# Kernel tuning notes

Measured on AMD Instinct MI355X. Metric: run time of the kernel, lower is better.

The kernel has to match this reference:

```python
import jax, jax.numpy as jnp
import numpy as np

N_NODES = 200000
N_EDGES = 3200000
N_GRAPHS = 64
IN_DIM, HIDDEN, OUT_DIM = 128, 16, 64


def setup_inputs() -> dict:
    key = jax.random.key(0)
    ks = jax.random.split(key, 5)
    x = jax.random.normal(ks[0], (N_NODES, IN_DIM), dtype=jnp.float32)
    edge_index = jax.random.randint(ks[1], (2, N_EDGES), 0, N_NODES, dtype=jnp.int64)
    batch = jnp.sort(jax.random.randint(ks[2], (N_NODES,), 0, N_GRAPHS, dtype=jnp.int64))
    W1 = jax.random.normal(ks[3], (IN_DIM, HIDDEN), dtype=jnp.float32) * (1.0 / np.sqrt(IN_DIM))
    W2 = jax.random.normal(ks[4], (HIDDEN, OUT_DIM), dtype=jnp.float32) * (1.0 / np.sqrt(HIDDEN))
    b1 = jnp.zeros((HIDDEN,), jnp.float32)
    b2 = jnp.zeros((OUT_DIM,), jnp.float32)
    return {"x": x, "edge_index": edge_index, "batch": batch,
            "W1": W1, "b1": b1, "W2": W2, "b2": b2, "training": 0}


def _gcn_conv(x, W, b, row, col, n_nodes):
    # PyG GCNConv: add-self-loop symmetric normalization, transform then
    # gather-from-row / scatter-add-to-col.  (row, col) already include self-loops.
    h = x @ W                                             # [N, out]
    deg = jnp.zeros((n_nodes,), h.dtype).at[col].add(1.0)  # degree incl. self-loop (>=1)
    dinv = deg ** -0.5
    norm = dinv[row] * dinv[col]                          # [E+N]
    out = jnp.zeros((n_nodes, W.shape[1]), h.dtype).at[col].add(h[row] * norm[:, None])
    return out + b


def reference(x, edge_index, batch, W1, b1, W2, b2, training):
    n = x.shape[0]
    loops = jnp.arange(n, dtype=edge_index.dtype)
    row = jnp.concatenate([edge_index[0], loops])
    col = jnp.concatenate([edge_index[1], loops])
    h = _gcn_conv(x, W1, b1, row, col, n)
    h = jax.nn.relu(h)
    # F.dropout with training=False is identity (reference is deterministic)
    h = _gcn_conv(h, W2, b2, row, col, n)
    # per-graph sum pooling: replaces the Python torch.where loop
    graph_embeds = jax.ops.segment_sum(h, batch, num_segments=N_GRAPHS)
    return graph_embeds
```

## Files before the change

kernel.cpp:

```cpp
#include <hip/hip_runtime.h>


#define TPB 256
#define CHUNK 4096
#define BK_SHIFT 9
#define NPB 512

__device__ __forceinline__ float bf2f(unsigned short u) {
    union { unsigned int i; float f; } v; v.i = ((unsigned int)u) << 16; return v.f;
}
__device__ __forceinline__ unsigned short f2bf(float f) {
    union { float f; unsigned int i; } v; v.f = f;
    unsigned int r = v.i + 0x7fff + ((v.i >> 16) & 1);
    return (unsigned short)(r >> 16);
}

__global__ __launch_bounds__(TPB) void hist_kernel(const int* __restrict__ col,
                                                   int* __restrict__ counts,
                                                   int E, int nblk, int nbuck) {
    __shared__ int hist[512];
    int t = threadIdx.x;
    for (int i = t; i < nbuck; i += TPB) hist[i] = 0;
    __syncthreads();
    int e0 = blockIdx.x * CHUNK;
    for (int i = t; i < CHUNK; i += TPB) {
        int e = e0 + i;
        if (e < E) atomicAdd(&hist[col[e] >> BK_SHIFT], 1);
    }
    __syncthreads();
    for (int i = t; i < nbuck; i += TPB) counts[i * nblk + blockIdx.x] = hist[i];
}

__global__ __launch_bounds__(TPB) void scan1_kernel(const int* __restrict__ in,
                                                    int* __restrict__ out,
                                                    int* __restrict__ bsum, int L) {
    __shared__ int s[TPB];
    int t = threadIdx.x;
    int i = blockIdx.x * TPB + t;
    int d = (i < L) ? in[i] : 0;
    s[t] = d; __syncthreads();
    for (int off = 1; off < TPB; off <<= 1) {
        int v = (t >= off) ? s[t - off] : 0;
        __syncthreads();
        s[t] += v;
        __syncthreads();
    }
    if (i < L) out[i] = s[t] - d;
    if (t == TPB - 1) bsum[blockIdx.x] = s[t];
}

__global__ __launch_bounds__(1024) void scan2_kernel(int* __restrict__ bsum, int nb) {
    __shared__ int s[1024];
    int t = threadIdx.x;
    int i0 = t * 2, i1 = t * 2 + 1;
    int v0 = (i0 < nb) ? bsum[i0] : 0;
    int v1 = (i1 < nb) ? bsum[i1] : 0;
    int pv = v0 + v1;
    s[t] = pv; __syncthreads();
    for (int off = 1; off < 1024; off <<= 1) {
        int u = (t >= off) ? s[t - off] : 0;
        __syncthreads();
        s[t] += u;
        __syncthreads();
    }
    int exc = s[t] - pv;
    if (i0 < nb) bsum[i0] = exc;
    if (i1 < nb) bsum[i1] = exc + v0;
}

__device__ __forceinline__ int cbase_at(const int* counts, const int* bsum, int f) {
    return counts[f] + bsum[f >> 8];
}

__global__ __launch_bounds__(TPB) void s1c_gemm_kernel(
        const int* __restrict__ row, const int* __restrict__ col,
        const int* __restrict__ counts, const int* __restrict__ bsum,
        int E, int nblk, int nbuck,
        int* __restrict__ bucketed,
        const float* __restrict__ x, const float* __restrict__ W1,
        unsigned short* __restrict__ h1b, int N, int nbg) {
    __shared__ int cur[NPB];
    __shared__ float w1s[128 * 16];
    int b = (int)blockIdx.x, t = threadIdx.x;
    int M = min(nblk, nbg);
    int role, id;
    if (b < 2 * M) { role = b & 1; id = b >> 1; }
    else           { role = (nblk > nbg) ? 0 : 1; id = b - M; }

    if (role == 0) {
        for (int i = t; i < nbuck; i += TPB)
            cur[i] = cbase_at(counts, bsum, i * nblk + id);
        __syncthreads();
        int e0 = id * CHUNK;
        for (int i = t; i < CHUNK; i += TPB) {
            int e = e0 + i;
            if (e < E) {
                int c = col[e];
                int pos = atomicAdd(&cur[c >> BK_SHIFT], 1);
                bucketed[pos] = ((c & (NPB - 1)) << 18) | row[e];
            }
        }
        return;
    }
    for (int i = t; i < 128 * 16; i += TPB) w1s[i] = W1[i];
    __syncthreads();
    int n = id * TPB + t;
    if (n >= N) return;
    const float4* xr = (const float4*)(x + (size_t)n * 128);
    float acc[16];
#pragma unroll
    for (int k = 0; k < 16; ++k) acc[k] = 0.f;
#pragma unroll 1
    for (int g = 0; g < 8; g += 2) {
        float4 vA0 = xr[g * 4 + 0], vA1 = xr[g * 4 + 1];
        float4 vA2 = xr[g * 4 + 2], vA3 = xr[g * 4 + 3];
        float4 vB0 = xr[g * 4 + 4], vB1 = xr[g * 4 + 5];
        float4 vB2 = xr[g * 4 + 6], vB3 = xr[g * 4 + 7];
        float xva[16] = {vA0.x, vA0.y, vA0.z, vA0.w, vA1.x, vA1.y, vA1.z, vA1.w,
                         vA2.x, vA2.y, vA2.z, vA2.w, vA3.x, vA3.y, vA3.z, vA3.w};
        float xvb[16] = {vB0.x, vB0.y, vB0.z, vB0.w, vB1.x, vB1.y, vB1.z, vB1.w,
                         vB2.x, vB2.y, vB2.z, vB2.w, vB3.x, vB3.y, vB3.z, vB3.w};
#pragma unroll
        for (int cc = 0; cc < 16; ++cc) {
            const float4* w4 = (const float4*)&w1s[(g * 16 + cc) * 16];
            float4 wa = w4[0], wb = w4[1], wc = w4[2], wd = w4[3];
            float xc = xva[cc];
            acc[0]  = fmaf(xc, wa.x, acc[0]);  acc[1]  = fmaf(xc, wa.y, acc[1]);
            acc[2]  = fmaf(xc, wa.z, acc[2]);  acc[3]  = fmaf(xc, wa.w, acc[3]);
            acc[4]  = fmaf(xc, wb.x, acc[4]);  acc[5]  = fmaf(xc, wb.y, acc[5]);
            acc[6]  = fmaf(xc, wb.z, acc[6]);  acc[7]  = fmaf(xc, wb.w, acc[7]);
            acc[8]  = fmaf(xc, wc.x, acc[8]);  acc[9]  = fmaf(xc, wc.y, acc[9]);
            acc[10] = fmaf(xc, wc.z, acc[10]); acc[11] = fmaf(xc, wc.w, acc[11]);
            acc[12] = fmaf(xc, wd.x, acc[12]); acc[13] = fmaf(xc, wd.y, acc[13]);
            acc[14] = fmaf(xc, wd.z, acc[14]); acc[15] = fmaf(xc, wd.w, acc[15]);
        }
#pragma unroll
        for (int cc = 0; cc < 16; ++cc) {
            const float4* w4 = (const float4*)&w1s[((g + 1) * 16 + cc) * 16];
            float4 wa = w4[0], wb = w4[1], wc = w4[2], wd = w4[3];
            float xc = xvb[cc];
            acc[0]  = fmaf(xc, wa.x, acc[0]);  acc[1]  = fmaf(xc, wa.y, acc[1]);
            acc[2]  = fmaf(xc, wa.z, acc[2]);  acc[3]  = fmaf(xc, wa.w, acc[3]);
            acc[4]  = fmaf(xc, wb.x, acc[4]);  acc[5]  = fmaf(xc, wb.y, acc[5]);
            acc[6]  = fmaf(xc, wb.z, acc[6]);  acc[7]  = fmaf(xc, wb.w, acc[7]);
            acc[8]  = fmaf(xc, wc.x, acc[8]);  acc[9]  = fmaf(xc, wc.y, acc[9]);
            acc[10] = fmaf(xc, wc.z, acc[10]); acc[11] = fmaf(xc, wc.w, acc[11]);
            acc[12] = fmaf(xc, wd.x, acc[12]); acc[13] = fmaf(xc, wd.y, acc[13]);
            acc[14] = fmaf(xc, wd.z, acc[14]); acc[15] = fmaf(xc, wd.w, acc[15]);
        }
    }
    unsigned int u[8];
#pragma unroll
    for (int j = 0; j < 8; ++j)
        u[j] = (unsigned int)f2bf(acc[2 * j]) | ((unsigned int)f2bf(acc[2 * j + 1]) << 16);
    uint4* o = (uint4*)(h1b + (size_t)n * 16);
    o[0] = make_uint4(u[0], u[1], u[2], u[3]);
    o[1] = make_uint4(u[4], u[5], u[6], u[7]);
}

__global__ __launch_bounds__(TPB) void sort_kernel(
        const int* __restrict__ bucketed,
        const int* __restrict__ counts, const int* __restrict__ bsum,
        int E, int nblk, int nbuck,
        int* __restrict__ csr, int* __restrict__ offs, float* __restrict__ dinv,
        const unsigned short* __restrict__ h1b, unsigned short* __restrict__ h1p, int N) {
    __shared__ int lhist[NPB];
    __shared__ int part[TPB];
    __shared__ float sdinv[NPB];
    int bk = blockIdx.x, t = threadIdx.x;
    int n0 = bk << BK_SHIFT;
    int n1 = min(n0 + NPB, N);
    int e0 = cbase_at(counts, bsum, bk * nblk);
    int e1 = (bk + 1 < nbuck) ? cbase_at(counts, bsum, (bk + 1) * nblk) : E;

    lhist[t] = 0; lhist[t + TPB] = 0;
    __syncthreads();
    for (int i = e0 + t; i < e1; i += TPB)
        atomicAdd(&lhist[bucketed[i] >> 18], 1);
    __syncthreads();

    int base = t * 2;
    int c0 = lhist[base], c1 = lhist[base + 1];
    int s = c0 + c1;
    part[t] = s;
    __syncthreads();
    for (int off = 1; off < TPB; off <<= 1) {
        int v = (t >= off) ? part[t - off] : 0;
        __syncthreads();
        part[t] += v;
        __syncthreads();
    }
    int o0 = e0 + part[t] - s;
    int o1 = o0 + c0;
    lhist[base] = o0; lhist[base + 1] = o1;
    sdinv[base]     = rsqrtf((float)c0 + 1.0f);
    sdinv[base + 1] = rsqrtf((float)c1 + 1.0f);
    int n = n0 + base;
    if (n + 0 < N) { offs[n + 0] = o0; dinv[n + 0] = sdinv[base]; }
    if (n + 1 < N) { offs[n + 1] = o1; dinv[n + 1] = sdinv[base + 1]; }
    __syncthreads();

    for (int i = e0 + t; i < e1; i += TPB) {
        int v = bucketed[i];
        int pos = atomicAdd(&lhist[v >> 18], 1);
        csr[pos] = v & 0x3FFFF;
    }
    int nq = (n1 - n0) * 4;
    for (int i = t; i < nq; i += TPB) {
        float dv = sdinv[i >> 2];
        uint2 u = ((const uint2*)h1b)[(size_t)n0 * 4 + i];
        float f0 = bf2f((unsigned short)(u.x & 0xffff));
        float f1 = bf2f((unsigned short)(u.x >> 16));
        float f2 = bf2f((unsigned short)(u.y & 0xffff));
        float f3 = bf2f((unsigned short)(u.y >> 16));
        ((ushort4*)h1p)[(size_t)n0 * 4 + i] =
            make_ushort4(f2bf(f0 * dv), f2bf(f1 * dv), f2bf(f2 * dv), f2bf(f3 * dv));
    }
    if (bk == 0 && t == 0) offs[N] = E;
}

__global__ __launch_bounds__(TPB) void gather1_kernel(const int* __restrict__ csr,
                                                      const int* __restrict__ offs,
                                                      const unsigned short* __restrict__ h1p,
                                                      const float* __restrict__ dinv,
                                                      const float* __restrict__ b1,
                                                      unsigned short* __restrict__ h2p, int N) {
    int t = threadIdx.x;
    int c = blockIdx.x * 16 + (t >> 4);
    int lane = t & 15;
    int half = lane >> 3;
    int kk = lane & 7;
    if (c >= N) return;
    int p0 = offs[c], p1 = offs[c + 1];
    float a0 = 0.f, a1 = 0.f;
    for (int p = p0; p < p1; p += 32) {
        int s_lo = csr[min(p + lane, p1 - 1)];
        int s_hi = csr[min(p + 16 + lane, p1 - 1)];
        int rem = p1 - p;
        unsigned int u[16];
#pragma unroll
        for (int j = 0; j < 8; ++j) {
            int sj = __shfl(s_lo, 2 * j + half, 16);
            u[j] = *(const unsigned int*)&h1p[(size_t)sj * 16 + 2 * kk];
        }
#pragma unroll
        for (int j = 8; j < 16; ++j) {
            int sj = __shfl(s_hi, 2 * j + half - 16, 16);
            u[j] = *(const unsigned int*)&h1p[(size_t)sj * 16 + 2 * kk];
        }
#pragma unroll
        for (int j = 0; j < 16; ++j) {
            bool ok = (2 * j + half) < rem;
            a0 += ok ? bf2f((unsigned short)(u[j] & 0xffff)) : 0.f;
            a1 += ok ? bf2f((unsigned short)(u[j] >> 16)) : 0.f;
        }
    }
    a0 += __shfl_xor(a0, 8, 16);
    a1 += __shfl_xor(a1, 8, 16);
    if (half == 0) {
        float dc = dinv[c];
        unsigned int us = *(const unsigned int*)&h1p[(size_t)c * 16 + 2 * kk];
        float s0 = bf2f((unsigned short)(us & 0xffff));
        float s1 = bf2f((unsigned short)(us >> 16));
        float r0 = fmaf(dc, a0 + s0, b1[2 * kk]);
        float r1 = fmaf(dc, a1 + s1, b1[2 * kk + 1]);
        r0 = dc * fmaxf(r0, 0.f);
        r1 = dc * fmaxf(r1, 0.f);
        unsigned int w = (unsigned int)f2bf(r0) | ((unsigned int)f2bf(r1) << 16);
        *(unsigned int*)&h2p[(size_t)c * 16 + 2 * kk] = w;
    }
}

__global__ __launch_bounds__(TPB) void gather2f_kernel(
        const int* __restrict__ csr, const int* __restrict__ offs,
        const unsigned short* __restrict__ h2p, const float* __restrict__ dinv,
        const float* __restrict__ W2, const float* __restrict__ b2,
        const int* __restrict__ batch, float* __restrict__ out, int N) {
    __shared__ float w2s[16 * 64];
    __shared__ float asT[64 * 17];
    __shared__ float pool[64];
    int t = threadIdx.x;
    for (int i = t; i < 16 * 64; i += TPB) w2s[i] = W2[i];
    if (t < 64) pool[t] = 0.f;

    int n0 = blockIdx.x * 64;
    int nLast = min(n0 + 63, N - 1);
    int g0 = batch[n0];
    bool uniform = (batch[nLast] == g0);

    int grp = t >> 4, lane = t & 15;
    int half = lane >> 3, kk = lane & 7;
#pragma unroll 1
    for (int it = 0; it < 4; ++it) {
        int m = grp * 4 + it;
        int c = n0 + m;
        if (c < N) {
            int p0 = offs[c], p1 = offs[c + 1];
            float a0 = 0.f, a1 = 0.f;
            for (int p = p0; p < p1; p += 32) {
                int s_lo = csr[min(p + lane, p1 - 1)];
                int s_hi = csr[min(p + 16 + lane, p1 - 1)];
                int rem = p1 - p;
                unsigned int u[16];
#pragma unroll
                for (int j = 0; j < 8; ++j) {
                    int sj = __shfl(s_lo, 2 * j + half, 16);
                    u[j] = *(const unsigned int*)&h2p[(size_t)sj * 16 + 2 * kk];
                }
#pragma unroll
                for (int j = 8; j < 16; ++j) {
                    int sj = __shfl(s_hi, 2 * j + half - 16, 16);
                    u[j] = *(const unsigned int*)&h2p[(size_t)sj * 16 + 2 * kk];
                }
#pragma unroll
                for (int j = 0; j < 16; ++j) {
                    bool ok = (2 * j + half) < rem;
                    a0 += ok ? bf2f((unsigned short)(u[j] & 0xffff)) : 0.f;
                    a1 += ok ? bf2f((unsigned short)(u[j] >> 16)) : 0.f;
                }
            }
            a0 += __shfl_xor(a0, 8, 16);
            a1 += __shfl_xor(a1, 8, 16);
            if (half == 0) {
                float dc = dinv[c];
                unsigned int us = *(const unsigned int*)&h2p[(size_t)c * 16 + 2 * kk];
                float s0 = bf2f((unsigned short)(us & 0xffff));
                float s1 = bf2f((unsigned short)(us >> 16));
                asT[m * 17 + 2 * kk]     = dc * (a0 + s0);
                asT[m * 17 + 2 * kk + 1] = dc * (a1 + s1);
            }
        }
    }
    __syncthreads();

    int wave = t >> 6, j = t & 63;
    float w2reg[16];
#pragma unroll
    for (int kx = 0; kx < 16; ++kx) w2reg[kx] = w2s[kx * 64 + j];
    float b2j = b2[j];
    float val = 0.f;
    int g_cur = -1;
#pragma unroll 1
    for (int mi = 0; mi < 16; ++mi) {
        int m = wave * 16 + mi;
        int c = n0 + m;
        if (c >= N) break;
        const float* ar = &asT[m * 17];
        float y = b2j;
#pragma unroll
        for (int kx = 0; kx < 16; ++kx) y = fmaf(ar[kx], w2reg[kx], y);
        if (uniform) {
            val += y;
        } else {
            int g = batch[c];
            if (g != g_cur) {
                if (g_cur >= 0) atomicAdd(&out[(size_t)g_cur * 64 + j], val);
                val = 0.f;
                g_cur = g;
            }
            val += y;
        }
    }
    if (uniform) {
        atomicAdd(&pool[j], val);
        __syncthreads();
        if (t < 64) atomicAdd(&out[(size_t)g0 * 64 + t], pool[t]);
    } else {
        if (g_cur >= 0) atomicAdd(&out[(size_t)g_cur * 64 + j], val);
    }
}

static inline size_t align64(size_t v) { return (v + 63) & ~(size_t)63; }

extern "C" void kernel_launch(void* const* d_in, const int* in_sizes, int n_in,
                              void* d_out, int out_size, void* d_ws, size_t ws_size,
                              hipStream_t stream) {
    const float* x     = (const float*)d_in[0];
    const int*   ei    = (const int*)d_in[1];
    const int*   batch = (const int*)d_in[2];
    const float* W1    = (const float*)d_in[3];
    const float* b1    = (const float*)d_in[4];
    const float* W2    = (const float*)d_in[5];
    const float* b2    = (const float*)d_in[6];

    const int N = in_sizes[0] / 128;
    const int E = in_sizes[1] / 2;
    const int* row = ei;
    const int* col = ei + E;

    const int NBLK  = (E + CHUNK - 1) / CHUNK;
    const int NBUCK = (N + NPB - 1) / NPB;
    const int L     = NBUCK * NBLK;
    const int NBS   = (L + TPB - 1) / TPB;
    const int NBG   = (N + TPB - 1) / TPB;

    char* p = (char*)d_ws;
    int*            counts   = (int*)p;            p += align64((size_t)L * 4);
    int*            bsum     = (int*)p;            p += align64(2048 * 4);
    int*            bucketed = (int*)p;            p += align64((size_t)E * 4);
    int*            csr      = (int*)p;            p += align64((size_t)E * 4);
    int*            offs     = (int*)p;            p += align64((size_t)(N + 1) * 4);
    float*          dinv     = (float*)p;          p += align64((size_t)N * 4);
    unsigned short* h1b      = (unsigned short*)p; p += align64((size_t)N * 16 * 2);
    unsigned short* h1p      = (unsigned short*)p; p += align64((size_t)N * 16 * 2);
    unsigned short* h2p      = (unsigned short*)p; p += align64((size_t)N * 16 * 2);
    float*          out      = (float*)d_out;

    hipMemsetAsync(out, 0, (size_t)out_size * sizeof(float), stream);

    hist_kernel<<<NBLK, TPB, 0, stream>>>(col, counts, E, NBLK, NBUCK);
    scan1_kernel<<<NBS, TPB, 0, stream>>>(counts, counts, bsum, L);
    scan2_kernel<<<1, 1024, 0, stream>>>(bsum, NBS);
    s1c_gemm_kernel<<<NBLK + NBG, TPB, 0, stream>>>(row, col, counts, bsum,
                                                    E, NBLK, NBUCK,
                                                    bucketed, x, W1, h1b, N, NBG);
    sort_kernel<<<NBUCK, TPB, 0, stream>>>(bucketed, counts, bsum, E, NBLK, NBUCK,
                                           csr, offs, dinv, h1b, h1p, N);
    gather1_kernel<<<(N + 15) / 16, TPB, 0, stream>>>(csr, offs, h1p, dinv, b1, h2p, N);
    gather2f_kernel<<<(N + 63) / 64, TPB, 0, stream>>>(csr, offs, h2p, dinv,
                                                       W2, b2, batch, out, N);
}
```

Baseline: 357.0 us.

## Locally sort edge chunk before bucket scatter and software-pipeline GEMM x loads

```diff
diff --git a/kernel.cpp b/kernel.cpp
--- a/kernel.cpp
+++ b/kernel.cpp
@@ -72,14 +72,39 @@
     return counts[f] + bsum[f >> 8];
 }
 
-__global__ __launch_bounds__(TPB) void s1c_gemm_kernel(
+#define GEMM_W16(XV, GB)                                                          \
+    {                                                                             \
+        _Pragma("unroll")                                                         \
+        for (int cc = 0; cc < 16; ++cc) {                                         \
+            const float4* w4 = (const float4*)&w1s[((GB) * 16 + cc) * 16];        \
+            float4 wa = w4[0], wb = w4[1], wc = w4[2], wd = w4[3];                \
+            float xc = (XV)[cc];                                                  \
+            acc[0]  = fmaf(xc, wa.x, acc[0]);  acc[1]  = fmaf(xc, wa.y, acc[1]);  \
+            acc[2]  = fmaf(xc, wa.z, acc[2]);  acc[3]  = fmaf(xc, wa.w, acc[3]);  \
+            acc[4]  = fmaf(xc, wb.x, acc[4]);  acc[5]  = fmaf(xc, wb.y, acc[5]);  \
+            acc[6]  = fmaf(xc, wb.z, acc[6]);  acc[7]  = fmaf(xc, wb.w, acc[7]);  \
+            acc[8]  = fmaf(xc, wc.x, acc[8]);  acc[9]  = fmaf(xc, wc.y, acc[9]);  \
+            acc[10] = fmaf(xc, wc.z, acc[10]); acc[11] = fmaf(xc, wc.w, acc[11]); \
+            acc[12] = fmaf(xc, wd.x, acc[12]); acc[13] = fmaf(xc, wd.y, acc[13]); \
+            acc[14] = fmaf(xc, wd.z, acc[14]); acc[15] = fmaf(xc, wd.w, acc[15]); \
+        }                                                                         \
+    }
+
+#define XV16(v0, v1, v2, v3)                                          \
+    { v0.x, v0.y, v0.z, v0.w, v1.x, v1.y, v1.z, v1.w,                 \
+      v2.x, v2.y, v2.z, v2.w, v3.x, v3.y, v3.z, v3.w }
+
+__global__ __launch_bounds__(TPB, 4) void s1c_gemm_kernel(
         const int* __restrict__ row, const int* __restrict__ col,
         const int* __restrict__ counts, const int* __restrict__ bsum,
         int E, int nblk, int nbuck,
         int* __restrict__ bucketed,
         const float* __restrict__ x, const float* __restrict__ W1,
         unsigned short* __restrict__ h1b, int N, int nbg) {
-    __shared__ int cur[NPB];
+    __shared__ int lhist[512];
+    __shared__ int gd[512];
+    __shared__ int part[TPB];
+    __shared__ unsigned short sidx[CHUNK];
     __shared__ float w1s[128 * 16];
     int b = (int)blockIdx.x, t = threadIdx.x;
     int M = min(nblk, nbg);
@@ -88,17 +113,40 @@
     else           { role = (nblk > nbg) ? 0 : 1; id = b - M; }
 
     if (role == 0) {
-        for (int i = t; i < nbuck; i += TPB)
-            cur[i] = cbase_at(counts, bsum, i * nblk + id);
-        __syncthreads();
         int e0 = id * CHUNK;
-        for (int i = t; i < CHUNK; i += TPB) {
-            int e = e0 + i;
-            if (e < E) {
-                int c = col[e];
-                int pos = atomicAdd(&cur[c >> BK_SHIFT], 1);
-                bucketed[pos] = ((c & (NPB - 1)) << 18) | row[e];
-            }
+        int nE = min(CHUNK, E - e0);
+        lhist[t] = 0; lhist[t + TPB] = 0;
+        __syncthreads();
+        for (int i = t; i < nE; i += TPB)
+            atomicAdd(&lhist[col[e0 + i] >> BK_SHIFT], 1);
+        __syncthreads();
+        int b0i = 2 * t, b1i = 2 * t + 1;
+        int c0 = lhist[b0i], c1 = lhist[b1i];
+        int s = c0 + c1;
+        part[t] = s; __syncthreads();
+        for (int off = 1; off < TPB; off <<= 1) {
+            int v = (t >= off) ? part[t - off] : 0;
+            __syncthreads();
+            part[t] += v;
+            __syncthreads();
+        }
+        int o0 = part[t] - s;
+        int o1 = o0 + c0;
+        lhist[b0i] = o0; lhist[b1i] = o1;
+        if (b0i < nbuck) gd[b0i] = cbase_at(counts, bsum, b0i * nblk + id) - o0;
+        if (b1i < nbuck) gd[b1i] = cbase_at(counts, bsum, b1i * nblk + id) - o1;
+        __syncthreads();
+        for (int i = t; i < nE; i += TPB) {
+            int bk = col[e0 + i] >> BK_SHIFT;
+            int lp = atomicAdd(&lhist[bk], 1);
+            sidx[lp] = (unsigned short)i;
+        }
+        __syncthreads();
+        for (int j = t; j < nE; j += TPB) {
+            int i = sidx[j];
+            int c = col[e0 + i];
+            int r = row[e0 + i];
+            bucketed[gd[c >> BK_SHIFT] + j] = ((c & (NPB - 1)) << 18) | r;
         }
         return;
     }
@@ -110,44 +158,45 @@
     float acc[16];
 #pragma unroll
     for (int k = 0; k < 16; ++k) acc[k] = 0.f;
-#pragma unroll 1
-    for (int g = 0; g < 8; g += 2) {
-        float4 vA0 = xr[g * 4 + 0], vA1 = xr[g * 4 + 1];
-        float4 vA2 = xr[g * 4 + 2], vA3 = xr[g * 4 + 3];
-        float4 vB0 = xr[g * 4 + 4], vB1 = xr[g * 4 + 5];
-        float4 vB2 = xr[g * 4 + 6], vB3 = xr[g * 4 + 7];
-        float xva[16] = {vA0.x, vA0.y, vA0.z, vA0.w, vA1.x, vA1.y, vA1.z, vA1.w,
-                         vA2.x, vA2.y, vA2.z, vA2.w, vA3.x, vA3.y, vA3.z, vA3.w};
-        float xvb[16] = {vB0.x, vB0.y, vB0.z, vB0.w, vB1.x, vB1.y, vB1.z, vB1.w,
-                         vB2.x, vB2.y, vB2.z, vB2.w, vB3.x, vB3.y, vB3.z, vB3.w};
-#pragma unroll
-        for (int cc = 0; cc < 16; ++cc) {
-            const float4* w4 = (const float4*)&w1s[(g * 16 + cc) * 16];
-            float4 wa = w4[0], wb = w4[1], wc = w4[2], wd = w4[3];
-            float xc = xva[cc];
-            acc[0]  = fmaf(xc, wa.x, acc[0]);  acc[1]  = fmaf(xc, wa.y, acc[1]);
-            acc[2]  = fmaf(xc, wa.z, acc[2]);  acc[3]  = fmaf(xc, wa.w, acc[3]);
-            acc[4]  = fmaf(xc, wb.x, acc[4]);  acc[5]  = fmaf(xc, wb.y, acc[5]);
-            acc[6]  = fmaf(xc, wb.z, acc[6]);  acc[7]  = fmaf(xc, wb.w, acc[7]);
-            acc[8]  = fmaf(xc, wc.x, acc[8]);  acc[9]  = fmaf(xc, wc.y, acc[9]);
-            acc[10] = fmaf(xc, wc.z, acc[10]); acc[11] = fmaf(xc, wc.w, acc[11]);
-            acc[12] = fmaf(xc, wd.x, acc[12]); acc[13] = fmaf(xc, wd.y, acc[13]);
-            acc[14] = fmaf(xc, wd.z, acc[14]); acc[15] = fmaf(xc, wd.w, acc[15]);
-        }
-#pragma unroll
-        for (int cc = 0; cc < 16; ++cc) {
-            const float4* w4 = (const float4*)&w1s[((g + 1) * 16 + cc) * 16];
-            float4 wa = w4[0], wb = w4[1], wc = w4[2], wd = w4[3];
-            float xc = xvb[cc];
-            acc[0]  = fmaf(xc, wa.x, acc[0]);  acc[1]  = fmaf(xc, wa.y, acc[1]);
-            acc[2]  = fmaf(xc, wa.z, acc[2]);  acc[3]  = fmaf(xc, wa.w, acc[3]);
-            acc[4]  = fmaf(xc, wb.x, acc[4]);  acc[5]  = fmaf(xc, wb.y, acc[5]);
-            acc[6]  = fmaf(xc, wb.z, acc[6]);  acc[7]  = fmaf(xc, wb.w, acc[7]);
-            acc[8]  = fmaf(xc, wc.x, acc[8]);  acc[9]  = fmaf(xc, wc.y, acc[9]);
-            acc[10] = fmaf(xc, wc.z, acc[10]); acc[11] = fmaf(xc, wc.w, acc[11]);
-            acc[12] = fmaf(xc, wd.x, acc[12]); acc[13] = fmaf(xc, wd.y, acc[13]);
-            acc[14] = fmaf(xc, wd.z, acc[14]); acc[15] = fmaf(xc, wd.w, acc[15]);
-        }
+    float4 p00 = xr[0],  p01 = xr[1],  p02 = xr[2],  p03 = xr[3];
+    float4 p10 = xr[4],  p11 = xr[5],  p12 = xr[6],  p13 = xr[7];
+    float4 p20 = xr[8],  p21 = xr[9],  p22 = xr[10], p23 = xr[11];
+    float4 p30 = xr[12], p31 = xr[13], p32 = xr[14], p33 = xr[15];
+    {
+        float xv[16] = XV16(p00, p01, p02, p03);
+        p00 = xr[16]; p01 = xr[17]; p02 = xr[18]; p03 = xr[19];
+        GEMM_W16(xv, 0);
+    }
+    {
+        float xv[16] = XV16(p10, p11, p12, p13);
+        p10 = xr[20]; p11 = xr[21]; p12 = xr[22]; p13 = xr[23];
+        GEMM_W16(xv, 1);
+    }
+    {
+        float xv[16] = XV16(p20, p21, p22, p23);
+        p20 = xr[24]; p21 = xr[25]; p22 = xr[26]; p23 = xr[27];
+        GEMM_W16(xv, 2);
+    }
+    {
+        float xv[16] = XV16(p30, p31, p32, p33);
+        p30 = xr[28]; p31 = xr[29]; p32 = xr[30]; p33 = xr[31];
+        GEMM_W16(xv, 3);
+    }
+    {
+        float xv[16] = XV16(p00, p01, p02, p03);
+        GEMM_W16(xv, 4);
+    }
+    {
+        float xv[16] = XV16(p10, p11, p12, p13);
+        GEMM_W16(xv, 5);
+    }
+    {
+        float xv[16] = XV16(p20, p21, p22, p23);
+        GEMM_W16(xv, 6);
+    }
+    {
+        float xv[16] = XV16(p30, p31, p32, p33);
+        GEMM_W16(xv, 7);
     }
     unsigned int u[8];
 #pragma unroll
```

New measurement: 351.8 us. Within noise of the previous version (-1.5%).
